# Optimization experiments

Measured on AMD Instinct MI355X. Metric: run time of the kernel, lower is better.

Reference implementation:

```python
import jax, jax.numpy as jnp
import numpy as np

B, S, H = 32, 2048, 1024


def sparsemax(z, axis):
    # Martins & Astudillo (2016) sparsemax projection onto the simplex.
    n = z.shape[axis]
    z_sorted = -jnp.sort(-z, axis=axis)  # descending sort
    z_cum = jnp.cumsum(z_sorted, axis=axis)
    k = jnp.arange(1, n + 1, dtype=z.dtype).reshape(
        [n if i == (axis % z.ndim) else 1 for i in range(z.ndim)])
    support = (1.0 + k * z_sorted) > z_cum
    k_z = jnp.sum(support, axis=axis, keepdims=True)  # support size per row
    tau = (jnp.take_along_axis(z_cum, k_z.astype(jnp.int32) - 1, axis=axis) - 1.0) / k_z.astype(z.dtype)
    return jnp.maximum(z - tau, 0.0)


def setup_inputs() -> dict:
    key = jax.random.key(0)
    ks = jax.random.split(key, 8)
    s = 1.0 / np.sqrt(H)
    return {
        "encoder_output": jax.random.normal(ks[0], (B, S, H), jnp.float32),
        "decoder_hidden": jax.random.normal(ks[1], (B, H), jnp.float32),
        "Wa_w": jax.random.uniform(ks[2], (H, H), jnp.float32, -s, s),
        "Wa_b": jax.random.uniform(ks[3], (H,), jnp.float32, -s, s),
        "Ua_w": jax.random.uniform(ks[4], (H, H), jnp.float32, -s, s),
        "Ua_b": jax.random.uniform(ks[5], (H,), jnp.float32, -s, s),
        "Va_w": jax.random.uniform(ks[6], (1, H), jnp.float32, -s, s),
        "Va_b": jax.random.uniform(ks[7], (1,), jnp.float32, -s, s),
    }


def reference(encoder_output, decoder_hidden, Wa_w, Wa_b, Ua_w, Ua_b, Va_w, Va_b):
    # query: [B, 1, H]
    query = (decoder_hidden @ Wa_w.T + Wa_b)[:, None, :]
    # keys: [B, S, H]
    keys = jnp.einsum('bsh,oh->bso', encoder_output, Ua_w) + Ua_b
    # energy: [B, S]
    energy = jnp.einsum('bsh,h->bs', jnp.tanh(keys + query), Va_w[0]) + Va_b[0]
    attention_weights = sparsemax(energy, axis=1)  # [B, S]
    # context: [B, 1, H]
    context = jnp.einsum('bs,bsh->bh', attention_weights, encoder_output)[:, None, :]
    return (context, attention_weights)
```

## Files before the change

kernel.cpp:

```cpp
#include <hip/hip_runtime.h>
#include <stdint.h>
#include <stddef.h>

#define BB 32
#define SS 2048
#define HH 1024
#define MTOT (BB*SS)

typedef _Float16 h8 __attribute__((ext_vector_type(8)));
typedef float f32x4 __attribute__((ext_vector_type(4)));

__device__ __forceinline__ void gload_lds16(const void* g, void* l) {
  __builtin_amdgcn_global_load_lds(
      (const __attribute__((address_space(1))) void*)g,
      (__attribute__((address_space(3))) void*)l,
      16, 0, 0);
}

__device__ __forceinline__ float fast_tanh(float x) {
  x = fminf(15.f, fmaxf(-15.f, x));
  float t = __expf(2.f * x);
  return (t - 1.f) * __builtin_amdgcn_rcpf(t + 1.f);
}

__global__ __launch_bounds__(256) void cvt_h(const float* __restrict__ src,
                                             _Float16* __restrict__ dst) {
  int t = blockIdx.x * 256 + threadIdx.x;
  const float4* s4 = (const float4*)src + (size_t)t * 2;
  float4 f0 = s4[0], f1 = s4[1];
  h8 v;
  v[0]=(_Float16)f0.x; v[1]=(_Float16)f0.y; v[2]=(_Float16)f0.z; v[3]=(_Float16)f0.w;
  v[4]=(_Float16)f1.x; v[5]=(_Float16)f1.y; v[6]=(_Float16)f1.z; v[7]=(_Float16)f1.w;
  *(h8*)(dst + (size_t)t * 8) = v;
}

__global__ __launch_bounds__(256) void query_k(const float* __restrict__ dh,
                                               const float* __restrict__ Wa,
                                               const float* __restrict__ Wa_b,
                                               const float* __restrict__ Ua_b,
                                               float* __restrict__ qv) {
  int gw = (blockIdx.x * 256 + threadIdx.x) >> 6;
  int lane = threadIdx.x & 63;
  int o = gw >> 5;
  int b = gw & 31;
  const float4* x4 = (const float4*)(dh + (size_t)b * HH);
  const float4* w4 = (const float4*)(Wa + (size_t)o * HH);
  float s = 0.f;
#pragma unroll
  for (int j = 0; j < 4; ++j) {
    float4 a = x4[lane + 64 * j];
    float4 c = w4[lane + 64 * j];
    s += a.x * c.x + a.y * c.y + a.z * c.z + a.w * c.w;
  }
#pragma unroll
  for (int d = 32; d >= 1; d >>= 1) s += __shfl_xor(s, d, 64);
  if (lane == 0) qv[b * HH + o] = s + Wa_b[o] + Ua_b[o];
}

template<bool AH>
__global__ __launch_bounds__(256) void energy_gemm(const float* __restrict__ Ag,
                                                   const _Float16* __restrict__ Ahp,
                                                   const _Float16* __restrict__ Bh,
                                                   const float* __restrict__ qv,
                                                   const float* __restrict__ Va,
                                                   float* __restrict__ energy) {
  __shared__ __align__(16) _Float16 As[128 * 64];
  __shared__ __align__(16) _Float16 Bs[128 * 64];

  const int tid  = threadIdx.x;
  const int lane = tid & 63;
  const int w    = tid >> 6;
  const int wrow = (w & 1) * 64;
  const int wcol = (w >> 1) * 64;
  const int lr   = lane & 15;
  const int lq   = lane >> 4;

  const int x     = blockIdx.x;
  const int xcd   = x & 7;
  const int i6    = x >> 3;
  const int strip = xcd * 64 + (i6 >> 3);
  const int nblk  = i6 & 7;
  const int m0    = strip * 128;
  const int n0    = nblk * 128;

  f32x4 acc[4][4];
#pragma unroll
  for (int i = 0; i < 4; ++i)
#pragma unroll
    for (int j = 0; j < 4; ++j) acc[i][j] = (f32x4){0.f, 0.f, 0.f, 0.f};

  for (int kt = 0; kt < 16; ++kt) {
    const int k0 = kt * 64;
#pragma unroll
    for (int i = 0; i < 4; ++i) {
      int g = tid + 256 * i;
      int r = g >> 3;
      int c = (g & 7) ^ (r & 7);
      gload_lds16(Bh + (size_t)(n0 + r) * HH + k0 + c * 8, &Bs[g * 8]);
    }
    if constexpr (AH) {
#pragma unroll
      for (int i = 0; i < 4; ++i) {
        int g = tid + 256 * i;
        int r = g >> 3;
        int c = (g & 7) ^ (r & 7);
        gload_lds16(Ahp + (size_t)(m0 + r) * HH + k0 + c * 8, &As[g * 8]);
      }
    } else {
      float4 fa[8];
#pragma unroll
      for (int i = 0; i < 4; ++i) {
        int g = tid + 256 * i;
        int r = g >> 3;
        int c = (g & 7) ^ (r & 7);
        const float* src = Ag + (size_t)(m0 + r) * HH + k0 + c * 8;
        fa[2 * i]     = *(const float4*)src;
        fa[2 * i + 1] = *(const float4*)(src + 4);
      }
#pragma unroll
      for (int i = 0; i < 4; ++i) {
        int g = tid + 256 * i;
        h8 v;
        v[0]=(_Float16)fa[2*i].x;   v[1]=(_Float16)fa[2*i].y;
        v[2]=(_Float16)fa[2*i].z;   v[3]=(_Float16)fa[2*i].w;
        v[4]=(_Float16)fa[2*i+1].x; v[5]=(_Float16)fa[2*i+1].y;
        v[6]=(_Float16)fa[2*i+1].z; v[7]=(_Float16)fa[2*i+1].w;
        *(h8*)&As[g * 8] = v;
      }
    }
    __syncthreads();
#pragma unroll
    for (int kk = 0; kk < 2; ++kk) {
      h8 af[4], bf[4];
#pragma unroll
      for (int i = 0; i < 4; ++i) {
        int ra = wrow + i * 16 + lr;
        int ca = kk * 4 + lq;
        af[i] = *(const h8*)&As[(ra * 8 + (ca ^ (ra & 7))) * 8];
        int rb = wcol + i * 16 + lr;
        bf[i] = *(const h8*)&Bs[(rb * 8 + (ca ^ (rb & 7))) * 8];
      }
#pragma unroll
      for (int i = 0; i < 4; ++i)
#pragma unroll
        for (int j = 0; j < 4; ++j)
          acc[i][j] = __builtin_amdgcn_mfma_f32_16x16x32_f16(af[i], bf[j], acc[i][j], 0, 0, 0);
    }
    __syncthreads();
  }

  const int bq = m0 >> 11;
  float qvv[4], vaw[4];
#pragma unroll
  for (int j = 0; j < 4; ++j) {
    int n = n0 + wcol + j * 16 + lr;
    qvv[j] = qv[bq * HH + n];
    vaw[j] = Va[n];
  }
#pragma unroll
  for (int i = 0; i < 4; ++i) {
    float p[4] = {0.f, 0.f, 0.f, 0.f};
#pragma unroll
    for (int j = 0; j < 4; ++j)
#pragma unroll
      for (int r = 0; r < 4; ++r)
        p[r] += fast_tanh(acc[i][j][r] + qvv[j]) * vaw[j];
#pragma unroll
    for (int r = 0; r < 4; ++r) {
      float v = p[r];
      v += __shfl_xor(v, 1, 64);
      v += __shfl_xor(v, 2, 64);
      v += __shfl_xor(v, 4, 64);
      v += __shfl_xor(v, 8, 64);
      if (lr == 0) {
        int m = m0 + wrow + i * 16 + lq * 4 + r;
        atomicAdd(&energy[m], v);
      }
    }
  }
}

__global__ __launch_bounds__(256) void spctx(const float* __restrict__ energy,
                                             const float* __restrict__ enc,
                                             const float* __restrict__ Va_b,
                                             float* __restrict__ ctx,
                                             float* __restrict__ attn) {
  const int b = blockIdx.x;
  const int tid = threadIdx.x;
  const int lane = tid & 63;
  const int w = tid >> 6;
  __shared__ float aval[SS];
  __shared__ int   sidx[SS];
  __shared__ int   cnt;
  if (tid == 0) cnt = 0;

  const float* z = energy + (size_t)b * SS;
  const float vb = Va_b[0];
  float zv[32];
#pragma unroll
  for (int k = 0; k < 32; ++k) zv[k] = z[lane + 64 * k] + vb;

  float mx = zv[0];
#pragma unroll
  for (int k = 1; k < 32; ++k) mx = fmaxf(mx, zv[k]);
#pragma unroll
  for (int d = 32; d >= 1; d >>= 1) mx = fmaxf(mx, __shfl_xor(mx, d, 64));

  float lo = mx - 1.f, hi = mx;
  for (int it = 0; it < 40; ++it) {
    float tau = 0.5f * (lo + hi);
    float ss = 0.f;
#pragma unroll
    for (int k = 0; k < 32; ++k) ss += fmaxf(zv[k] - tau, 0.f);
#pragma unroll
    for (int d = 32; d >= 1; d >>= 1) ss += __shfl_xor(ss, d, 64);
    if (ss >= 1.f) lo = tau; else hi = tau;
  }
  const float tau = 0.5f * (lo + hi);

  __syncthreads();
#pragma unroll
  for (int kk = 0; kk < 8; ++kk) {
    int k = w * 8 + kk;
    int s = lane + 64 * k;
    float a = fmaxf(zv[k] - tau, 0.f);
    attn[(size_t)b * SS + s] = a;
    if (a > 0.f) {
      int p = atomicAdd(&cnt, 1);
      sidx[p] = s;
      aval[p] = a;
    }
  }
  __syncthreads();

  const int n = cnt;
  float c0 = 0.f, c1 = 0.f, c2 = 0.f, c3 = 0.f;
  const float* eb = enc + (size_t)b * SS * HH;
  for (int p = 0; p < n; ++p) {
    float a = aval[p];
    const float* row = eb + (size_t)sidx[p] * HH;
    c0 += a * row[tid];
    c1 += a * row[tid + 256];
    c2 += a * row[tid + 512];
    c3 += a * row[tid + 768];
  }
  ctx[(size_t)b * HH + tid]       = c0;
  ctx[(size_t)b * HH + tid + 256] = c1;
  ctx[(size_t)b * HH + tid + 512] = c2;
  ctx[(size_t)b * HH + tid + 768] = c3;
}

extern "C" void kernel_launch(void* const* d_in, const int* in_sizes, int n_in,
                              void* d_out, int out_size, void* d_ws, size_t ws_size,
                              hipStream_t stream) {
  const float* enc  = (const float*)d_in[0];
  const float* dh   = (const float*)d_in[1];
  const float* Wa_w = (const float*)d_in[2];
  const float* Wa_b = (const float*)d_in[3];
  const float* Ua_w = (const float*)d_in[4];
  const float* Ua_b = (const float*)d_in[5];
  const float* Va_w = (const float*)d_in[6];
  const float* Va_b = (const float*)d_in[7];

  float* out_ctx  = (float*)d_out;
  float* out_attn = (float*)d_out + BB * HH;

  char* ws = (char*)d_ws;
  _Float16* Ua_h = (_Float16*)ws;
  float* qv      = (float*)(ws + 2 * 1024 * 1024);
  float* energy  = (float*)(ws + 2 * 1024 * 1024 + 128 * 1024);
  _Float16* enc_h = (_Float16*)(ws + 4 * 1024 * 1024);

  const size_t need_h = 4ull * 1024 * 1024 + (size_t)MTOT * HH * sizeof(_Float16);
  const bool use_ah = (ws_size >= need_h);

  if (use_ah) {
    cvt_h<<<32768, 256, 0, stream>>>(enc, enc_h);
  }
  cvt_h<<<512, 256, 0, stream>>>(Ua_w, Ua_h);
  query_k<<<8192, 256, 0, stream>>>(dh, Wa_w, Wa_b, Ua_b, qv);
  hipMemsetAsync(energy, 0, MTOT * sizeof(float), stream);
  if (use_ah) {
    energy_gemm<true><<<4096, 256, 0, stream>>>(enc, enc_h, Ua_h, qv, Va_w, energy);
  } else {
    energy_gemm<false><<<4096, 256, 0, stream>>>(enc, nullptr, Ua_h, qv, Va_w, energy);
  }
  spctx<<<32, 256, 0, stream>>>(energy, enc, Va_b, out_ctx, out_attn);
}
```

Baseline: 641.6 us.

## Fuse fp16 conversion into energy GEMM with per-row-strip blocks and double buffering

After: 756.6 us. 1.18x slower.

```diff
diff --git a/kernel.cpp b/kernel.cpp
--- a/kernel.cpp
+++ b/kernel.cpp
@@ -57,15 +57,14 @@
   if (lane == 0) qv[b * HH + o] = s + Wa_b[o] + Ua_b[o];
 }
 
-template<bool AH>
-__global__ __launch_bounds__(256) void energy_gemm(const float* __restrict__ Ag,
-                                                   const _Float16* __restrict__ Ahp,
-                                                   const _Float16* __restrict__ Bh,
-                                                   const float* __restrict__ qv,
-                                                   const float* __restrict__ Va,
-                                                   float* __restrict__ energy) {
-  __shared__ __align__(16) _Float16 As[128 * 64];
-  __shared__ __align__(16) _Float16 Bs[128 * 64];
+__global__ __launch_bounds__(256) void energy_fused(const float* __restrict__ Ag,
+                                                    _Float16* __restrict__ slotb,
+                                                    const _Float16* __restrict__ Bh,
+                                                    const float* __restrict__ qv,
+                                                    const float* __restrict__ Va,
+                                                    float* __restrict__ energy) {
+  __shared__ __align__(16) _Float16 As[2][128 * 64];
+  __shared__ __align__(16) _Float16 Bs[2][128 * 64];
 
   const int tid  = threadIdx.x;
   const int lane = tid & 63;
@@ -74,7 +73,148 @@
   const int wcol = (w >> 1) * 64;
   const int lr   = lane & 15;
   const int lq   = lane >> 4;
-
+  const int m0   = blockIdx.x * 128;
+
+  const float* src  = Ag + (size_t)m0 * HH;
+  _Float16*    slot = slotb + (size_t)m0 * HH;
+  for (int it = 0; it < 64; ++it) {
+    int off = it * 2048 + tid * 8;
+    float4 f0 = *(const float4*)(src + off);
+    float4 f1 = *(const float4*)(src + off + 4);
+    h8 v;
+    v[0]=(_Float16)f0.x; v[1]=(_Float16)f0.y; v[2]=(_Float16)f0.z; v[3]=(_Float16)f0.w;
+    v[4]=(_Float16)f1.x; v[5]=(_Float16)f1.y; v[6]=(_Float16)f1.z; v[7]=(_Float16)f1.w;
+    *(h8*)(slot + off) = v;
+  }
+  __threadfence();
+  __syncthreads();
+
+  f32x4 acc[4][4];
+  float es[4][4];
+#pragma unroll
+  for (int i = 0; i < 4; ++i)
+#pragma unroll
+    for (int r = 0; r < 4; ++r) es[i][r] = 0.f;
+
+  const int bq = m0 >> 11;
+
+#define STAGE(buf, nb_, kt_) do {                                              \
+    const int k0_ = (kt_) * 64;                                                \
+    _Pragma("unroll")                                                          \
+    for (int i_ = 0; i_ < 4; ++i_) {                                           \
+      int g_ = tid + 256 * i_;                                                 \
+      int r_ = g_ >> 3;                                                        \
+      int c_ = (g_ & 7) ^ (r_ & 7);                                            \
+      gload_lds16(Bh + (size_t)((nb_) * 128 + r_) * HH + k0_ + c_ * 8,         \
+                  &Bs[buf][g_ * 8]);                                           \
+      gload_lds16(slot + (size_t)r_ * HH + k0_ + c_ * 8, &As[buf][g_ * 8]);    \
+    }                                                                          \
+  } while (0)
+
+  STAGE(0, 0, 0);
+  __syncthreads();
+  int cur = 0;
+
+  for (int t = 0; t < 128; ++t) {
+    const int nb = t >> 4;
+    const int kt = t & 15;
+    if (kt == 0) {
+#pragma unroll
+      for (int i = 0; i < 4; ++i)
+#pragma unroll
+        for (int j = 0; j < 4; ++j) acc[i][j] = (f32x4){0.f, 0.f, 0.f, 0.f};
+    }
+    if (t + 1 < 128) {
+      const int t1 = t + 1;
+      STAGE(cur ^ 1, t1 >> 4, t1 & 15);
+    }
+    (void)kt;
+#pragma unroll
+    for (int kk = 0; kk < 2; ++kk) {
+      h8 af[4], bf[4];
+#pragma unroll
+      for (int i = 0; i < 4; ++i) {
+        int ra = wrow + i * 16 + lr;
+        int ca = kk * 4 + lq;
+        af[i] = *(const h8*)&As[cur][(ra * 8 + (ca ^ (ra & 7))) * 8];
+        int rb = wcol + i * 16 + lr;
+        bf[i] = *(const h8*)&Bs[cur][(rb * 8 + (ca ^ (rb & 7))) * 8];
+      }
+#pragma unroll
+      for (int i = 0; i < 4; ++i)
+#pragma unroll
+        for (int j = 0; j < 4; ++j)
+          acc[i][j] = __builtin_amdgcn_mfma_f32_16x16x32_f16(af[i], bf[j], acc[i][j], 0, 0, 0);
+    }
+    if (kt == 15) {
+      float qvv[4], vaw[4];
+#pragma unroll
+      for (int j = 0; j < 4; ++j) {
+        int n = nb * 128 + wcol + j * 16 + lr;
+        qvv[j] = qv[bq * HH + n];
+        vaw[j] = Va[n];
+      }
+#pragma unroll
+      for (int i = 0; i < 4; ++i) {
+        float p[4] = {0.f, 0.f, 0.f, 0.f};
+#pragma unroll
+        for (int j = 0; j < 4; ++j)
+#pragma unroll
+          for (int r = 0; r < 4; ++r)
+            p[r] += fast_tanh(acc[i][j][r] + qvv[j]) * vaw[j];
+#pragma unroll
+        for (int r = 0; r < 4; ++r) {
+          float v = p[r];
+          v += __shfl_xor(v, 1, 64);
+          v += __shfl_xor(v, 2, 64);
+          v += __shfl_xor(v, 4, 64);
+          v += __shfl_xor(v, 8, 64);
+          es[i][r] += v;
+        }
+      }
+    }
+    __syncthreads();
+    cur ^= 1;
+  }
+#undef STAGE
+
+  float* esh = (float*)As;
+  if (w >= 2) {
+#pragma unroll
+    for (int i = 0; i < 4; ++i)
+#pragma unroll
+      for (int r = 0; r < 4; ++r) esh[(tid - 128) * 16 + i * 4 + r] = es[i][r];
+  }
+  __syncthreads();
+  if (w < 2) {
+#pragma unroll
+    for (int i = 0; i < 4; ++i)
+#pragma unroll
+      for (int r = 0; r < 4; ++r) es[i][r] += esh[tid * 16 + i * 4 + r];
+    if (lr == 0) {
+#pragma unroll
+      for (int i = 0; i < 4; ++i)
+#pragma unroll
+        for (int r = 0; r < 4; ++r)
+          energy[m0 + wrow + i * 16 + lq * 4 + r] = es[i][r];
+    }
+  }
+}
+
+__global__ __launch_bounds__(256) void energy_gemm_f32(const float* __restrict__ Ag,
+                                                       const _Float16* __restrict__ Bh,
+                                                       const float* __restrict__ qv,
+                                                       const float* __restrict__ Va,
+                                                       float* __restrict__ energy) {
+  __shared__ __align__(16) _Float16 As[128 * 64];
+  __shared__ __align__(16) _Float16 Bs[128 * 64];
+  const int tid  = threadIdx.x;
+  const int lane = tid & 63;
+  const int w    = tid >> 6;
+  const int wrow = (w & 1) * 64;
+  const int wcol = (w >> 1) * 64;
+  const int lr   = lane & 15;
+  const int lq   = lane >> 4;
   const int x     = blockIdx.x;
   const int xcd   = x & 7;
   const int i6    = x >> 3;
@@ -82,13 +222,11 @@
   const int nblk  = i6 & 7;
   const int m0    = strip * 128;
   const int n0    = nblk * 128;
-
   f32x4 acc[4][4];
 #pragma unroll
   for (int i = 0; i < 4; ++i)
 #pragma unroll
     for (int j = 0; j < 4; ++j) acc[i][j] = (f32x4){0.f, 0.f, 0.f, 0.f};
-
   for (int kt = 0; kt < 16; ++kt) {
     const int k0 = kt * 64;
 #pragma unroll
@@ -98,35 +236,25 @@
       int c = (g & 7) ^ (r & 7);
       gload_lds16(Bh + (size_t)(n0 + r) * HH + k0 + c * 8, &Bs[g * 8]);
     }
-    if constexpr (AH) {
-#pragma unroll
-      for (int i = 0; i < 4; ++i) {
-        int g = tid + 256 * i;
-        int r = g >> 3;
-        int c = (g & 7) ^ (r & 7);
-        gload_lds16(Ahp + (size_t)(m0 + r) * HH + k0 + c * 8, &As[g * 8]);
-      }
-    } else {
-      float4 fa[8];
-#pragma unroll
-      for (int i = 0; i < 4; ++i) {
-        int g = tid + 256 * i;
-        int r = g >> 3;
-        int c = (g & 7) ^ (r & 7);
-        const float* src = Ag + (size_t)(m0 + r) * HH + k0 + c * 8;
-        fa[2 * i]     = *(const float4*)src;
-        fa[2 * i + 1] = *(const float4*)(src + 4);
-      }
-#pragma unroll
-      for (int i = 0; i < 4; ++i) {
-        int g = tid + 256 * i;
-        h8 v;
-        v[0]=(_Float16)fa[2*i].x;   v[1]=(_Float16)fa[2*i].y;
-        v[2]=(_Float16)fa[2*i].z;   v[3]=(_Float16)fa[2*i].w;
-        v[4]=(_Float16)fa[2*i+1].x; v[5]=(_Float16)fa[2*i+1].y;
-        v[6]=(_Float16)fa[2*i+1].z; v[7]=(_Float16)fa[2*i+1].w;
-        *(h8*)&As[g * 8] = v;
-      }
+    float4 fa[8];
+#pragma unroll
+    for (int i = 0; i < 4; ++i) {
+      int g = tid + 256 * i;
+      int r = g >> 3;
+      int c = (g & 7) ^ (r & 7);
+      const float* src = Ag + (size_t)(m0 + r) * HH + k0 + c * 8;
+      fa[2 * i]     = *(const float4*)src;
+      fa[2 * i + 1] = *(const float4*)(src + 4);
+    }
+#pragma unroll
+    for (int i = 0; i < 4; ++i) {
+      int g = tid + 256 * i;
+      h8 v;
+      v[0]=(_Float16)fa[2*i].x;   v[1]=(_Float16)fa[2*i].y;
+      v[2]=(_Float16)fa[2*i].z;   v[3]=(_Float16)fa[2*i].w;
+      v[4]=(_Float16)fa[2*i+1].x; v[5]=(_Float16)fa[2*i+1].y;
+      v[6]=(_Float16)fa[2*i+1].z; v[7]=(_Float16)fa[2*i+1].w;
+      *(h8*)&As[g * 8] = v;
     }
     __syncthreads();
 #pragma unroll
@@ -148,7 +276,6 @@
     }
     __syncthreads();
   }
-
   const int bq = m0 >> 11;
   float qvv[4], vaw[4];
 #pragma unroll
@@ -272,18 +399,15 @@
   _Float16* enc_h = (_Float16*)(ws + 4 * 1024 * 1024);
 
   const size_t need_h = 4ull * 1024 * 1024 + (size_t)MTOT * HH * sizeof(_Float16);
-  const bool use_ah = (ws_size >= need_h);
-
-  if (use_ah) {
-    cvt_h<<<32768, 256, 0, stream>>>(enc, enc_h);
-  }
+  const bool fits = (ws_size >= need_h);
+
   cvt_h<<<512, 256, 0, stream>>>(Ua_w, Ua_h);
   query_k<<<8192, 256, 0, stream>>>(dh, Wa_w, Wa_b, Ua_b, qv);
-  hipMemsetAsync(energy, 0, MTOT * sizeof(float), stream);
-  if (use_ah) {
-    energy_gemm<true><<<4096, 256, 0, stream>>>(enc, enc_h, Ua_h, qv, Va_w, energy);
+  if (fits) {
+    energy_fused<<<512, 256, 0, stream>>>(enc, enc_h, Ua_h, qv, Va_w, energy);
   } else {
-    energy_gemm<false><<<4096, 256, 0, stream>>>(enc, nullptr, Ua_h, qv, Va_w, energy);
+    hipMemsetAsync(energy, 0, MTOT * sizeof(float), stream);
+    energy_gemm_f32<<<4096, 256, 0, stream>>>(enc, Ua_h, qv, Va_w, energy);
   }
   spctx<<<32, 256, 0, stream>>>(energy, enc, Va_b, out_ctx, out_attn);
 }
```
